# Performance work log

Measured on AMD Instinct MI355X. Metric: run time of the kernel, lower is better.

Reference implementation:

```python
import jax, jax.numpy as jnp
import numpy as np

jax.config.update("jax_enable_x64", True)  # hash uses int64 multiply-xor like torch .long()

NUM_LEVELS = 16
LEVEL_DIM = 2
PER_LEVEL_SCALE = 2
BASE_RES = 16
LOG2_HASHMAP = 19
PS1 = 19349663  # second spatial hash prime (ps[0] == 1)
N_POINTS = 524288


def _isprime(n):
    for p in range(2, int(n ** 0.5) + 1):
        if n % p == 0:
            return False
    return True


N_ENTRIES = 2 ** LOG2_HASHMAP
while not _isprime(N_ENTRIES):
    N_ENTRIES += 1  # -> 524309

SCALES = []
OFFSETS = [0]
START_HASH = NUM_LEVELS  # module uses -1 sentinel; NUM_LEVELS == 'no hashing yet'
for i in range(NUM_LEVELS):
    res = int(BASE_RES * PER_LEVEL_SCALE ** i)
    SCALES.append(res)
    n = (res + 1) ** 2
    if n > N_ENTRIES:
        if START_HASH == NUM_LEVELS:
            START_HASH = i
        n = N_ENTRIES
    OFFSETS.append(OFFSETS[-1] + n)
TABLE_SIZE = OFFSETS[-1]  # 5594552

CORNERS = jnp.array([[0.0, 0.0], [0.0, 1.0], [1.0, 0.0], [1.0, 1.0]], dtype=jnp.float32)  # [4,2]
SCALES_F = jnp.array(SCALES, dtype=jnp.float32)          # [L]
SCALES_I = jnp.array(SCALES, dtype=jnp.int64)            # [L]
LEVEL_OFF = jnp.array(OFFSETS[:-1], dtype=jnp.int64)     # [L] base offset per level


def setup_inputs() -> dict:
    key = jax.random.key(0)
    k1, k2 = jax.random.split(key)
    x = jax.random.uniform(k1, (N_POINTS, 2), dtype=jnp.float32)  # coords in [0,1)
    data = (jax.random.uniform(k2, (TABLE_SIZE, LEVEL_DIM), dtype=jnp.float32) * 2.0 - 1.0) * 1e-4
    return {"x": x, "data": data}


def reference(x, data):
    L, F = NUM_LEVELS, LEVEL_DIM
    float_x = x[None] * SCALES_F[:, None, None]                                  # [L,N,2]
    int_x = (float_x[:, :, None, :] + CORNERS[None, None]).astype(jnp.int64)     # [L,N,4,2]
    offset_x = float_x - int_x[:, :, 0].astype(float_x.dtype)                    # [L,N,2] frac part
    ix0, ix1 = int_x[..., 0], int_x[..., 1]
    # dense-grid index for low levels, spatial hash for high levels
    grid_ind = ix0 * (SCALES_I + 1)[:, None, None] + ix1                         # [L,N,4]
    hash_ind = (ix0 ^ (ix1 * PS1)) % N_ENTRIES                                   # [L,N,4]
    is_grid = (jnp.arange(L) < START_HASH)[:, None, None]
    ind = jnp.where(is_grid, grid_ind, hash_ind) + LEVEL_OFF[:, None, None]      # [L,N,4]
    val = data[ind]                                                              # [L,N,4,F]
    # bilinear corner weights: clamp(1 - c + (2c-1)*frac) per axis, product over xy
    w = jnp.clip(1.0 - CORNERS[None, None] + (2.0 * CORNERS[None, None] - 1.0) * offset_x[:, :, None], 0.0, 1.0)
    w = w[..., 0] * w[..., 1]                                                    # [L,N,4]
    out = jnp.einsum('lnc,lncf->lnf', w, val)                                    # [L,N,F]
    return out.transpose(1, 0, 2).reshape(-1, L * F)                             # [N, L*F]
```

## Files before the change

kernel.cpp:

```cpp
#include <hip/hip_runtime.h>


static constexpr int  kPoints    = 524288;
static constexpr int  kLevels    = 16;
static constexpr int  kStartHash = 6;
static constexpr long long kPs1     = 19349663LL;
static constexpr long long kEntries = 524309LL;

__constant__ long long c_level_off[kLevels] = {
    0LL, 289LL, 1378LL, 5603LL, 22244LL, 88293LL, 351462LL,
    875771LL, 1400080LL, 1924389LL, 2448698LL, 2973007LL,
    3497316LL, 4021625LL, 4545934LL, 5070243LL
};

__device__ __forceinline__ float2 interp_level(
    const float2 p, const float2* __restrict__ tbl, const int l)
{
    const int   scale_i = 16 << l;
    const float scale_f = (float)scale_i;

    const float fx = p.x * scale_f;
    const float fy = p.y * scale_f;

    const long long ix0 = (long long)fx;
    const long long iy0 = (long long)fy;
    const long long ix1 = (long long)(fx + 1.0f);
    const long long iy1 = (long long)(fy + 1.0f);

    const float ox = fx - (float)ix0;
    const float oy = fy - (float)iy0;

    const float wx1 = fminf(fmaxf(ox, 0.0f), 1.0f);
    const float wx0 = fminf(fmaxf(1.0f - ox, 0.0f), 1.0f);
    const float wy1 = fminf(fmaxf(oy, 0.0f), 1.0f);
    const float wy0 = fminf(fmaxf(1.0f - oy, 0.0f), 1.0f);

    long long i00, i01, i10, i11;
    if (l < kStartHash) {
        const long long stride = (long long)(scale_i + 1);
        i00 = ix0 * stride + iy0;
        i01 = ix0 * stride + iy1;
        i10 = ix1 * stride + iy0;
        i11 = ix1 * stride + iy1;
    } else {
        const long long hy0 = iy0 * kPs1;
        const long long hy1 = iy1 * kPs1;
        i00 = (ix0 ^ hy0) % kEntries;
        i01 = (ix0 ^ hy1) % kEntries;
        i10 = (ix1 ^ hy0) % kEntries;
        i11 = (ix1 ^ hy1) % kEntries;
    }

    const long long base = c_level_off[l];
    const float2 v00 = tbl[base + i00];
    const float2 v01 = tbl[base + i01];
    const float2 v10 = tbl[base + i10];
    const float2 v11 = tbl[base + i11];

    const float w00 = wx0 * wy0;
    const float w01 = wx0 * wy1;
    const float w10 = wx1 * wy0;
    const float w11 = wx1 * wy1;

    return make_float2(
        w00 * v00.x + w01 * v01.x + w10 * v10.x + w11 * v11.x,
        w00 * v00.y + w01 * v01.y + w10 * v10.y + w11 * v11.y);
}

__global__ __launch_bounds__(256) void level_pass(
    const float2* __restrict__ x,
    const float2* __restrict__ tbl,
    float2* __restrict__ ws)
{
    const int b    = blockIdx.x;
    const int xcd  = b & 7;
    const int slot = b >> 3;

    int level, pblk;
    if (slot < 2048) {
        level = 6 + xcd;
        pblk  = slot;
    } else if (slot < 2304) {
        level = 14;
        pblk  = xcd * 256 + (slot - 2048);
    } else if (slot < 2560) {
        level = 15;
        pblk  = xcd * 256 + (slot - 2304);
    } else {
        const int d = xcd * 1536 + (slot - 2560);
        level = d >> 11;
        pblk  = d & 2047;
    }

    const int n = (pblk << 8) | threadIdx.x;
    const float2 p = x[n];
    ws[(size_t)level * kPoints + n] = interp_level(p, tbl, level);
}

static constexpr int kTStride = 257;

__global__ __launch_bounds__(256) void transpose_out(
    const float2* __restrict__ ws,
    float4* __restrict__ out)
{
    __shared__ float2 lds[kLevels * kTStride];

    const int t  = threadIdx.x;
    const int n0 = blockIdx.x * 256;

#pragma unroll
    for (int l = 0; l < kLevels; ++l)
        lds[l * kTStride + t] = ws[(size_t)l * kPoints + n0 + t];

    __syncthreads();

    float4* o = out + (size_t)n0 * 8;
#pragma unroll
    for (int k = 0; k < 8; ++k) {
        const int f  = k * 256 + t;
        const int nl = f >> 3;
        const int i  = t & 7;
        const float2 a = lds[(2 * i)     * kTStride + nl];
        const float2 b = lds[(2 * i + 1) * kTStride + nl];
        o[f] = make_float4(a.x, a.y, b.x, b.y);
    }
}

__global__ __launch_bounds__(256) void hashgrid_fwd(
    const float2* __restrict__ x,
    const float2* __restrict__ tbl,
    float4* __restrict__ out)
{
    const int n = blockIdx.x * blockDim.x + threadIdx.x;
    if (n >= kPoints) return;
    const float2 p = x[n];
    float acc[2 * kLevels];
#pragma unroll
    for (int l = 0; l < kLevels; ++l) {
        const float2 r = interp_level(p, tbl, l);
        acc[2 * l + 0] = r.x;
        acc[2 * l + 1] = r.y;
    }
    float4* o = out + (size_t)n * 8;
#pragma unroll
    for (int i = 0; i < 8; ++i)
        o[i] = make_float4(acc[4 * i + 0], acc[4 * i + 1],
                           acc[4 * i + 2], acc[4 * i + 3]);
}

extern "C" void kernel_launch(void* const* d_in, const int* in_sizes, int n_in,
                              void* d_out, int out_size, void* d_ws, size_t ws_size,
                              hipStream_t stream) {
    const float2* x   = (const float2*)d_in[0];
    const float2* tbl = (const float2*)d_in[1];

    const size_t ws_needed = (size_t)kLevels * kPoints * sizeof(float2);
    if (ws_size >= ws_needed) {
        float2* ws = (float2*)d_ws;
        level_pass<<<kLevels * (kPoints / 256), 256, 0, stream>>>(x, tbl, ws);
        transpose_out<<<kPoints / 256, 256, 0, stream>>>(ws, (float4*)d_out);
    } else {
        hashgrid_fwd<<<kPoints / 256, 256, 0, stream>>>(x, tbl, (float4*)d_out);
    }
}
```

Before: 227.0 us.

## Use 32-bit hash arithmetic, batch 4 points per thread, nontemporal workspace I/O

Replaces the 64-bit multiply, xor and modulo hash with a 32-bit decomposition (the high word folded in via 2^32 mod the table size), and switches indices to unsigned 32-bit. Each thread now processes four points per level so that sixteen independent gathers are in flight, and the block-to-level schedule is rescaled to match. Workspace and output writes, and the workspace reads, use nontemporal hints so the streamed data does not pollute cache that holds the hash table. The four-point batching raises register pressure, and the index math relies on the coordinates being non-negative.

Measured after the change: 233.4 us. 1.03x slower.

```diff
diff --git a/kernel.cpp b/kernel.cpp
--- a/kernel.cpp
+++ b/kernel.cpp
@@ -1,73 +1,32 @@
 #include <hip/hip_runtime.h>
 
 
-static constexpr int  kPoints    = 524288;
-static constexpr int  kLevels    = 16;
-static constexpr int  kStartHash = 6;
-static constexpr long long kPs1     = 19349663LL;
-static constexpr long long kEntries = 524309LL;
-
-__constant__ long long c_level_off[kLevels] = {
-    0LL, 289LL, 1378LL, 5603LL, 22244LL, 88293LL, 351462LL,
-    875771LL, 1400080LL, 1924389LL, 2448698LL, 2973007LL,
-    3497316LL, 4021625LL, 4545934LL, 5070243LL
+static constexpr int kPoints = 524288;
+static constexpr int kLevels = 16;
+
+__constant__ unsigned c_level_off[kLevels] = {
+    0u, 289u, 1378u, 5603u, 22244u, 88293u, 351462u,
+    875771u, 1400080u, 1924389u, 2448698u, 2973007u,
+    3497316u, 4021625u, 4545934u, 5070243u
 };
 
-__device__ __forceinline__ float2 interp_level(
-    const float2 p, const float2* __restrict__ tbl, const int l)
-{
-    const int   scale_i = 16 << l;
-    const float scale_f = (float)scale_i;
-
-    const float fx = p.x * scale_f;
-    const float fy = p.y * scale_f;
-
-    const long long ix0 = (long long)fx;
-    const long long iy0 = (long long)fy;
-    const long long ix1 = (long long)(fx + 1.0f);
-    const long long iy1 = (long long)(fy + 1.0f);
-
-    const float ox = fx - (float)ix0;
-    const float oy = fy - (float)iy0;
-
-    const float wx1 = fminf(fmaxf(ox, 0.0f), 1.0f);
-    const float wx0 = fminf(fmaxf(1.0f - ox, 0.0f), 1.0f);
-    const float wy1 = fminf(fmaxf(oy, 0.0f), 1.0f);
-    const float wy0 = fminf(fmaxf(1.0f - oy, 0.0f), 1.0f);
-
-    long long i00, i01, i10, i11;
-    if (l < kStartHash) {
-        const long long stride = (long long)(scale_i + 1);
-        i00 = ix0 * stride + iy0;
-        i01 = ix0 * stride + iy1;
-        i10 = ix1 * stride + iy0;
-        i11 = ix1 * stride + iy1;
-    } else {
-        const long long hy0 = iy0 * kPs1;
-        const long long hy1 = iy1 * kPs1;
-        i00 = (ix0 ^ hy0) % kEntries;
-        i01 = (ix0 ^ hy1) % kEntries;
-        i10 = (ix1 ^ hy0) % kEntries;
-        i11 = (ix1 ^ hy1) % kEntries;
-    }
-
-    const long long base = c_level_off[l];
-    const float2 v00 = tbl[base + i00];
-    const float2 v01 = tbl[base + i01];
-    const float2 v10 = tbl[base + i10];
-    const float2 v11 = tbl[base + i11];
-
-    const float w00 = wx0 * wy0;
-    const float w01 = wx0 * wy1;
-    const float w10 = wx1 * wy0;
-    const float w11 = wx1 * wy1;
-
-    return make_float2(
-        w00 * v00.x + w01 * v01.x + w10 * v10.x + w11 * v11.x,
-        w00 * v00.y + w01 * v01.y + w10 * v10.y + w11 * v11.y);
-}
-
-__global__ __launch_bounds__(256) void level_pass(
+typedef unsigned int v4u __attribute__((ext_vector_type(4)));
+
+__device__ __forceinline__ void nt_store_f2(float2* p, float2 v) {
+    union { float2 f; unsigned long long u; } c; c.f = v;
+    __builtin_nontemporal_store(c.u, (unsigned long long*)p);
+}
+__device__ __forceinline__ float2 nt_load_f2(const float2* p) {
+    union { float2 f; unsigned long long u; } c;
+    c.u = __builtin_nontemporal_load((const unsigned long long*)p);
+    return c.f;
+}
+__device__ __forceinline__ void nt_store_f4(float4* p, float4 v) {
+    union { float4 f; v4u u; } c; c.f = v;
+    __builtin_nontemporal_store(c.u, (v4u*)p);
+}
+
+__global__ __launch_bounds__(256) void level_pass4(
     const float2* __restrict__ x,
     const float2* __restrict__ tbl,
     float2* __restrict__ ws)
@@ -77,24 +36,82 @@
     const int slot = b >> 3;
 
     int level, pblk;
-    if (slot < 2048) {
+    if (slot < 512) {
         level = 6 + xcd;
         pblk  = slot;
-    } else if (slot < 2304) {
-        level = 14;
-        pblk  = xcd * 256 + (slot - 2048);
-    } else if (slot < 2560) {
-        level = 15;
-        pblk  = xcd * 256 + (slot - 2304);
+    } else if (slot < 576) {
+        level = 14;  pblk = xcd * 64 + (slot - 512);
+    } else if (slot < 640) {
+        level = 15;  pblk = xcd * 64 + (slot - 576);
     } else {
-        const int d = xcd * 1536 + (slot - 2560);
-        level = d >> 11;
-        pblk  = d & 2047;
-    }
-
-    const int n = (pblk << 8) | threadIdx.x;
-    const float2 p = x[n];
-    ws[(size_t)level * kPoints + n] = interp_level(p, tbl, level);
+        const int d = xcd * 384 + (slot - 640);
+        level = d >> 9;
+        pblk  = d & 511;
+    }
+
+    const int t  = threadIdx.x;
+    const int n0 = (pblk << 10) | t;
+
+    const int   scale_i = 16 << level;
+    const float scale_f = (float)scale_i;
+    const unsigned base = c_level_off[level];
+
+    float wx0[4], wx1[4], wy0[4], wy1[4];
+    unsigned idx[4][4];
+
+#pragma unroll
+    for (int k = 0; k < 4; ++k) {
+        const float2 p = x[n0 + (k << 8)];
+        const float fx = p.x * scale_f;
+        const float fy = p.y * scale_f;
+        const unsigned ix0 = (unsigned)(int)fx;
+        const unsigned iy0 = (unsigned)(int)fy;
+        const unsigned ix1 = ix0 + 1u;
+
+        const float ox = fx - (float)(int)ix0;
+        const float oy = fy - (float)(int)iy0;
+        wx1[k] = fminf(fmaxf(ox, 0.0f), 1.0f);
+        wx0[k] = fminf(fmaxf(1.0f - ox, 0.0f), 1.0f);
+        wy1[k] = fminf(fmaxf(oy, 0.0f), 1.0f);
+        wy0[k] = fminf(fmaxf(1.0f - oy, 0.0f), 1.0f);
+
+        if (level < 6) {
+            const unsigned stride = (unsigned)(scale_i + 1);
+            const unsigned i00 = ix0 * stride + iy0;
+            idx[k][0] = i00;
+            idx[k][1] = i00 + 1u;
+            idx[k][2] = i00 + stride;
+            idx[k][3] = i00 + stride + 1u;
+        } else {
+            const unsigned long long prod0 = (unsigned long long)iy0 * 19349663ull;
+            const unsigned long long prod1 = prod0 + 19349663ull;
+            const unsigned hi0 = (unsigned)(prod0 >> 32);
+            const unsigned lo0 = (unsigned)prod0;
+            const unsigned hi1 = (unsigned)(prod1 >> 32);
+            const unsigned lo1 = (unsigned)prod1;
+            idx[k][0] = (hi0 * 352277u + (lo0 ^ ix0) % 524309u) % 524309u;
+            idx[k][1] = (hi1 * 352277u + (lo1 ^ ix0) % 524309u) % 524309u;
+            idx[k][2] = (hi0 * 352277u + (lo0 ^ ix1) % 524309u) % 524309u;
+            idx[k][3] = (hi1 * 352277u + (lo1 ^ ix1) % 524309u) % 524309u;
+        }
+    }
+
+    float2 v[4][4];
+#pragma unroll
+    for (int k = 0; k < 4; ++k)
+#pragma unroll
+        for (int c = 0; c < 4; ++c)
+            v[k][c] = tbl[base + idx[k][c]];
+
+#pragma unroll
+    for (int k = 0; k < 4; ++k) {
+        const float w00 = wx0[k] * wy0[k], w01 = wx0[k] * wy1[k];
+        const float w10 = wx1[k] * wy0[k], w11 = wx1[k] * wy1[k];
+        float2 r;
+        r.x = w00 * v[k][0].x + w01 * v[k][1].x + w10 * v[k][2].x + w11 * v[k][3].x;
+        r.y = w00 * v[k][0].y + w01 * v[k][1].y + w10 * v[k][2].y + w11 * v[k][3].y;
+        nt_store_f2(&ws[(size_t)level * kPoints + n0 + (k << 8)], r);
+    }
 }
 
 static constexpr int kTStride = 257;
@@ -110,7 +127,7 @@
 
 #pragma unroll
     for (int l = 0; l < kLevels; ++l)
-        lds[l * kTStride + t] = ws[(size_t)l * kPoints + n0 + t];
+        lds[l * kTStride + t] = nt_load_f2(&ws[(size_t)l * kPoints + n0 + t]);
 
     __syncthreads();
 
@@ -122,7 +139,7 @@
         const int i  = t & 7;
         const float2 a = lds[(2 * i)     * kTStride + nl];
         const float2 b = lds[(2 * i + 1) * kTStride + nl];
-        o[f] = make_float4(a.x, a.y, b.x, b.y);
+        nt_store_f4(&o[f], make_float4(a.x, a.y, b.x, b.y));
     }
 }
 
@@ -137,9 +154,43 @@
     float acc[2 * kLevels];
 #pragma unroll
     for (int l = 0; l < kLevels; ++l) {
-        const float2 r = interp_level(p, tbl, l);
-        acc[2 * l + 0] = r.x;
-        acc[2 * l + 1] = r.y;
+        const int   scale_i = 16 << l;
+        const float scale_f = (float)scale_i;
+        const float fx = p.x * scale_f;
+        const float fy = p.y * scale_f;
+        const unsigned ix0 = (unsigned)(int)fx;
+        const unsigned iy0 = (unsigned)(int)fy;
+        const unsigned ix1 = ix0 + 1u;
+        const float ox = fx - (float)(int)ix0;
+        const float oy = fy - (float)(int)iy0;
+        const float wx1 = fminf(fmaxf(ox, 0.0f), 1.0f);
+        const float wx0 = fminf(fmaxf(1.0f - ox, 0.0f), 1.0f);
+        const float wy1 = fminf(fmaxf(oy, 0.0f), 1.0f);
+        const float wy0 = fminf(fmaxf(1.0f - oy, 0.0f), 1.0f);
+        unsigned i00, i01, i10, i11;
+        if (l < 6) {
+            const unsigned stride = (unsigned)(scale_i + 1);
+            i00 = ix0 * stride + iy0; i01 = i00 + 1u;
+            i10 = i00 + stride;       i11 = i10 + 1u;
+        } else {
+            const unsigned long long prod0 = (unsigned long long)iy0 * 19349663ull;
+            const unsigned long long prod1 = prod0 + 19349663ull;
+            const unsigned hi0 = (unsigned)(prod0 >> 32), lo0 = (unsigned)prod0;
+            const unsigned hi1 = (unsigned)(prod1 >> 32), lo1 = (unsigned)prod1;
+            i00 = (hi0 * 352277u + (lo0 ^ ix0) % 524309u) % 524309u;
+            i01 = (hi1 * 352277u + (lo1 ^ ix0) % 524309u) % 524309u;
+            i10 = (hi0 * 352277u + (lo0 ^ ix1) % 524309u) % 524309u;
+            i11 = (hi1 * 352277u + (lo1 ^ ix1) % 524309u) % 524309u;
+        }
+        const unsigned base = c_level_off[l];
+        const float2 v00 = tbl[base + i00];
+        const float2 v01 = tbl[base + i01];
+        const float2 v10 = tbl[base + i10];
+        const float2 v11 = tbl[base + i11];
+        const float w00 = wx0 * wy0, w01 = wx0 * wy1;
+        const float w10 = wx1 * wy0, w11 = wx1 * wy1;
+        acc[2 * l + 0] = w00 * v00.x + w01 * v01.x + w10 * v10.x + w11 * v11.x;
+        acc[2 * l + 1] = w00 * v00.y + w01 * v01.y + w10 * v10.y + w11 * v11.y;
     }
     float4* o = out + (size_t)n * 8;
 #pragma unroll
@@ -157,7 +208,7 @@
     const size_t ws_needed = (size_t)kLevels * kPoints * sizeof(float2);
     if (ws_size >= ws_needed) {
         float2* ws = (float2*)d_ws;
-        level_pass<<<kLevels * (kPoints / 256), 256, 0, stream>>>(x, tbl, ws);
+        level_pass4<<<kLevels * (kPoints / 1024), 256, 0, stream>>>(x, tbl, ws);
         transpose_out<<<kPoints / 256, 256, 0, stream>>>(ws, (float4*)d_out);
     } else {
         hashgrid_fwd<<<kPoints / 256, 256, 0, stream>>>(x, tbl, (float4*)d_out);
```
